# Optimization experiments

Measured on AMD Instinct MI355X. Metric: run time of the kernel, lower is better.

Reference implementation:

```python
import jax, jax.numpy as jnp
import numpy as np

N = 100000      # num_nodes
E = 1600000     # num_edges (avg degree 16)
IN = 128        # in_feats
OUT = 64        # out_feats
D = 4           # num_divisions


def setup_inputs() -> dict:
    key = jax.random.key(0)
    ks = jax.random.split(key, 6)
    feature = jax.random.normal(ks[0], (N, IN), dtype=jnp.float32)
    # per-division linear weights, stored as [D, out, in] (torch Linear layout)
    W = jax.random.normal(ks[1], (D, OUT, IN), dtype=jnp.float32) * (1.0 / np.sqrt(IN))
    norm = jax.random.uniform(ks[2], (N, 1), dtype=jnp.float32)
    src = jax.random.randint(ks[3], (E,), 0, N)
    dst = jax.random.randint(ks[4], (E,), 0, N)
    edge_div = jax.random.randint(ks[5], (E,), 0, D)
    return {"feature": feature, "W": W, "norm": norm,
            "src": src, "dst": dst, "edge_div": edge_div}


def reference(feature, W, norm, src, dst, edge_div):
    # Per-division linear transform + per-node norm scaling: [D, N, OUT]
    t = jnp.einsum('ni,doi->dno', feature, W) * norm
    # Gather the source-node features for each edge from its division's transform
    msgs = t[edge_div, src]                      # [E, OUT]
    # Scatter-sum to (dst, division) slots in one segment_sum pass
    seg = dst * D + edge_div                     # [E]
    agg = jax.ops.segment_sum(msgs, seg, num_segments=N * D)  # [N*D, OUT]
    # Row order is node-major, division-minor -> reshape == torch.cat over divisions
    h = agg.reshape(N, D * OUT) * norm           # final norm scale
    return jax.nn.relu(h)
```

## Files before the change

kernel.cpp:

```cpp
#include <hip/hip_runtime.h>


#define IN_F   128
#define OUTC   256
#define GM_ROWS 64
#define EPC    4096
#define NBMAX  512
#define STGF   5120

__device__ inline unsigned short f32_to_bf16(float f) {
    unsigned int u = __float_as_uint(f);
    unsigned int r = (u + 0x7FFFu + ((u >> 16) & 1u)) >> 16;
    return (unsigned short)r;
}
__device__ inline float bf16_to_f32(unsigned short h) {
    return __uint_as_float(((unsigned int)h) << 16);
}

__global__ __launch_bounds__(256) void transposeW_kernel(
    const float* __restrict__ W, float* __restrict__ Wt)
{
    const int idx = blockIdx.x * 256 + threadIdx.x;
    const int c = idx >> 7;
    const int k = idx & 127;
    Wt[k * OUTC + c] = W[idx];
}

__global__ __launch_bounds__(256) void gemm_kernel(
    const float* __restrict__ feat, const float* __restrict__ Wt,
    const float* __restrict__ norm, unsigned short* __restrict__ t, int nNodes)
{
    __shared__ float As[128][GM_ROWS + 4];

    const int tid = threadIdx.x;
    const int m0 = blockIdx.x * GM_ROWS;

    #pragma unroll
    for (int it = 0; it < 8; ++it) {
        const int idx = it * 1024 + tid * 4;
        const int row = idx >> 7;
        const int col = idx & 127;
        float4 v = make_float4(0.f, 0.f, 0.f, 0.f);
        const int g = m0 + row;
        if (g < nNodes) v = *(const float4*)(feat + (size_t)g * IN_F + col);
        As[col + 0][row] = v.x; As[col + 1][row] = v.y;
        As[col + 2][row] = v.z; As[col + 3][row] = v.w;
    }
    __syncthreads();

    const int tx = tid & 31;
    const int ty = tid >> 5;
    const int mb = ty * 8, nb = tx * 8;
    float acc[8][8] = {};

    #pragma unroll 4
    for (int k = 0; k < 128; ++k) {
        const float4 a0 = *(const float4*)&As[k][mb];
        const float4 a1 = *(const float4*)&As[k][mb + 4];
        const float4 b0 = *(const float4*)(Wt + k * OUTC + nb);
        const float4 b1 = *(const float4*)(Wt + k * OUTC + nb + 4);
        const float a[8] = {a0.x, a0.y, a0.z, a0.w, a1.x, a1.y, a1.z, a1.w};
        const float b[8] = {b0.x, b0.y, b0.z, b0.w, b1.x, b1.y, b1.z, b1.w};
        #pragma unroll
        for (int i = 0; i < 8; ++i)
            #pragma unroll
            for (int j = 0; j < 8; ++j)
                acc[i][j] = fmaf(a[i], b[j], acc[i][j]);
    }

    #pragma unroll
    for (int i = 0; i < 8; ++i) {
        const int gm = m0 + mb + i;
        if (gm >= nNodes) continue;
        const float nm = norm[gm];
        union { unsigned short u[8]; uint4 v; } o;
        #pragma unroll
        for (int j = 0; j < 8; ++j) o.u[j] = f32_to_bf16(acc[i][j] * nm);
        *(uint4*)(t + (size_t)gm * OUTC + nb) = o.v;
    }
}

__global__ __launch_bounds__(256) void bucket_hist_kernel(
    const int* __restrict__ dst, int* __restrict__ bcnt, int nEdges, int nBuck)
{
    __shared__ int h[NBMAX];
    const int tid = threadIdx.x;
    for (int b = tid; b < nBuck; b += 256) h[b] = 0;
    __syncthreads();
    const int e0 = blockIdx.x * EPC;
    const int cnt = min(EPC, nEdges - e0);
    for (int i = tid; i < cnt; i += 256)
        atomicAdd(&h[((unsigned)dst[e0 + i]) >> 8], 1);
    __syncthreads();
    for (int b = tid; b < nBuck; b += 256)
        if (h[b]) atomicAdd(&bcnt[b], h[b]);
}

__global__ __launch_bounds__(256) void bucket_scan_kernel(
    const int* __restrict__ bcnt, int* __restrict__ bbase,
    int* __restrict__ bfront, int nBuck)
{
    __shared__ int wsum[4], woff[4];
    const int tid = threadIdx.x;
    const int i0 = 2 * tid, i1 = 2 * tid + 1;
    const int h0 = (i0 < nBuck) ? bcnt[i0] : 0;
    const int h1 = (i1 < nBuck) ? bcnt[i1] : 0;
    const int s = h0 + h1;
    int incl = s;
    const int lane = tid & 63;
    #pragma unroll
    for (int off = 1; off < 64; off <<= 1) {
        const int o = __shfl_up(incl, off);
        if (lane >= off) incl += o;
    }
    if (lane == 63) wsum[tid >> 6] = incl;
    __syncthreads();
    if (tid == 0) { int r = 0; for (int i = 0; i < 4; ++i) { woff[i] = r; r += wsum[i]; } }
    __syncthreads();
    const int e = incl - s + woff[tid >> 6];
    if (i0 < nBuck) { bbase[i0] = e;      bfront[i0] = e;      }
    if (i1 < nBuck) { bbase[i1] = e + h0; bfront[i1] = e + h0; }
}

__global__ __launch_bounds__(256) void bucket_place_kernel(
    const int* __restrict__ src, const int* __restrict__ dst,
    const int* __restrict__ ediv, int* __restrict__ bfront,
    uint2* __restrict__ rec, int nEdges, int nBuck)
{
    __shared__ uint2 stg[EPC];
    __shared__ unsigned short stgB[EPC];
    __shared__ int hist[NBMAX], excl[NBMAX], cur[NBMAX], gpos[NBMAX];
    __shared__ int wsum[4], woff[4];

    const int tid = threadIdx.x;
    const int e0 = blockIdx.x * EPC;
    const int cnt = min(EPC, nEdges - e0);

    for (int b = tid; b < nBuck; b += 256) hist[b] = 0;
    __syncthreads();

    for (int i = tid; i < cnt; i += 256)
        atomicAdd(&hist[((unsigned)dst[e0 + i]) >> 8], 1);
    __syncthreads();

    {
        const int i0 = 2 * tid, i1 = 2 * tid + 1;
        const int h0 = (i0 < nBuck) ? hist[i0] : 0;
        const int h1 = (i1 < nBuck) ? hist[i1] : 0;
        const int s = h0 + h1;
        int incl = s;
        const int lane = tid & 63;
        #pragma unroll
        for (int off = 1; off < 64; off <<= 1) {
            const int o = __shfl_up(incl, off);
            if (lane >= off) incl += o;
        }
        if (lane == 63) wsum[tid >> 6] = incl;
        __syncthreads();
        if (tid == 0) { int r = 0; for (int i = 0; i < 4; ++i) { woff[i] = r; r += wsum[i]; } }
        __syncthreads();
        const int e = incl - s + woff[tid >> 6];
        if (i0 < nBuck) { excl[i0] = e;      cur[i0] = e;
                          gpos[i0] = h0 ? atomicAdd(&bfront[i0], h0) : 0; }
        if (i1 < nBuck) { excl[i1] = e + h0; cur[i1] = e + h0;
                          gpos[i1] = h1 ? atomicAdd(&bfront[i1], h1) : 0; }
    }
    __syncthreads();

    for (int i = tid; i < cnt; i += 256) {
        const int e = e0 + i;
        const int d = dst[e];
        const int b = ((unsigned)d) >> 8;
        const int lp = atomicAdd(&cur[b], 1);
        stg[lp]  = make_uint2((unsigned)((src[e] << 2) | ediv[e]), (unsigned)d);
        stgB[lp] = (unsigned short)b;
    }
    __syncthreads();

    for (int s2 = tid; s2 < cnt; s2 += 256) {
        const int b = stgB[s2];
        rec[gpos[b] + (s2 - excl[b])] = stg[s2];
    }
}

__global__ __launch_bounds__(256) void bucket_fine_kernel(
    const uint2* __restrict__ rec, const int* __restrict__ bbase,
    const int* __restrict__ bcnt, int* __restrict__ cursor,
    int* __restrict__ payload, int nNodes)
{
    __shared__ int nhist[256], ncur[256];
    __shared__ int pay[STGF];
    __shared__ int wsum[4], woff[4];

    const int tid = threadIdx.x;
    const int b = blockIdx.x;
    const int base = bbase[b];
    const int cnt = bcnt[b];
    const int node0 = b << 8;

    nhist[tid] = 0;
    __syncthreads();
    for (int i = tid; i < cnt; i += 256)
        atomicAdd(&nhist[rec[base + i].y & 255], 1);
    __syncthreads();

    const int v = nhist[tid];
    int incl = v;
    const int lane = tid & 63;
    #pragma unroll
    for (int off = 1; off < 64; off <<= 1) {
        const int o = __shfl_up(incl, off);
        if (lane >= off) incl += o;
    }
    if (lane == 63) wsum[tid >> 6] = incl;
    __syncthreads();
    if (tid == 0) { int r = 0; for (int i = 0; i < 4; ++i) { woff[i] = r; r += wsum[i]; } }
    __syncthreads();
    incl += woff[tid >> 6];
    ncur[tid] = incl - v;
    if (node0 + tid < nNodes) cursor[node0 + tid] = base + incl;
    __syncthreads();

    if (cnt <= STGF) {
        for (int i = tid; i < cnt; i += 256) {
            const uint2 r = rec[base + i];
            pay[atomicAdd(&ncur[r.y & 255], 1)] = (int)r.x;
        }
        __syncthreads();
        for (int i = tid; i < cnt; i += 256) payload[base + i] = pay[i];
    } else {
        for (int i = tid; i < cnt; i += 256) {
            const uint2 r = rec[base + i];
            payload[base + atomicAdd(&ncur[r.y & 255], 1)] = (int)r.x;
        }
    }
}

__global__ __launch_bounds__(256) void aggregate_kernel(
    const unsigned short* __restrict__ t, const int* __restrict__ cursor,
    const int* __restrict__ payload, const float* __restrict__ norm,
    float* __restrict__ out, int nNodes)
{
    const int wave = (int)((blockIdx.x * 256u + threadIdx.x) >> 6);
    const int lane = threadIdx.x & 63;
    if (wave >= nNodes) return;
    const int e0 = (wave == 0) ? 0 : cursor[wave - 1];
    const int e1 = cursor[wave];

    float acc0 = 0.f, acc1 = 0.f, acc2 = 0.f, acc3 = 0.f;
    int e = e0;
    for (; e + 1 < e1; e += 2) {
        const int p0 = payload[e];
        const int p1 = payload[e + 1];
        const float v0 = bf16_to_f32(t[(size_t)(p0 >> 2) * OUTC + (p0 & 3) * 64 + lane]);
        const float v1 = bf16_to_f32(t[(size_t)(p1 >> 2) * OUTC + (p1 & 3) * 64 + lane]);
        const int d0 = p0 & 3, d1 = p1 & 3;
        acc0 += (d0 == 0 ? v0 : 0.f) + (d1 == 0 ? v1 : 0.f);
        acc1 += (d0 == 1 ? v0 : 0.f) + (d1 == 1 ? v1 : 0.f);
        acc2 += (d0 == 2 ? v0 : 0.f) + (d1 == 2 ? v1 : 0.f);
        acc3 += (d0 == 3 ? v0 : 0.f) + (d1 == 3 ? v1 : 0.f);
    }
    if (e < e1) {
        const int p0 = payload[e];
        const float v0 = bf16_to_f32(t[(size_t)(p0 >> 2) * OUTC + (p0 & 3) * 64 + lane]);
        const int d0 = p0 & 3;
        acc0 += (d0 == 0 ? v0 : 0.f);
        acc1 += (d0 == 1 ? v0 : 0.f);
        acc2 += (d0 == 2 ? v0 : 0.f);
        acc3 += (d0 == 3 ? v0 : 0.f);
    }

    const float nm = norm[wave];
    float* po = out + (size_t)wave * OUTC;
    po[0 * 64 + lane] = fmaxf(acc0 * nm, 0.f);
    po[1 * 64 + lane] = fmaxf(acc1 * nm, 0.f);
    po[2 * 64 + lane] = fmaxf(acc2 * nm, 0.f);
    po[3 * 64 + lane] = fmaxf(acc3 * nm, 0.f);
}

extern "C" void kernel_launch(void* const* d_in, const int* in_sizes, int n_in,
                              void* d_out, int out_size, void* d_ws, size_t ws_size,
                              hipStream_t stream) {
    const float* feat = (const float*)d_in[0];
    const float* W    = (const float*)d_in[1];
    const float* norm = (const float*)d_in[2];
    const int*   src  = (const int*)d_in[3];
    const int*   dst  = (const int*)d_in[4];
    const int*   ediv = (const int*)d_in[5];
    float* out = (float*)d_out;

    const int nNodes = in_sizes[0] / IN_F;
    const int nEdges = in_sizes[3];
    const int nBuck  = (nNodes + 255) >> 8;
    const int nChunk = (nEdges + EPC - 1) / EPC;

    char* ws = (char*)d_ws;
    const size_t t_bytes      = (size_t)nNodes * OUTC * sizeof(unsigned short);
    const size_t rec_bytes    = (size_t)nEdges * sizeof(uint2);
    const size_t pay_bytes    = (size_t)nEdges * sizeof(int);
    const size_t cursor_bytes = (size_t)nNodes * sizeof(int);
    const size_t wt_bytes     = (size_t)IN_F * OUTC * sizeof(float);
    const size_t bk_bytes     = (size_t)NBMAX * sizeof(int);

    unsigned short* t  = (unsigned short*)ws;
    uint2* rec     = (uint2*)(ws + t_bytes);
    int*   payload = (int*)(ws + t_bytes + rec_bytes);
    int*   cursor  = (int*)(ws + t_bytes + rec_bytes + pay_bytes);
    float* Wt      = (float*)(ws + t_bytes + rec_bytes + pay_bytes + cursor_bytes);
    int*   bcnt    = (int*)(ws + t_bytes + rec_bytes + pay_bytes + cursor_bytes + wt_bytes);
    int*   bbase   = bcnt + NBMAX;
    int*   bfront  = bcnt + 2 * NBMAX;
    (void)ws_size; (void)out_size; (void)n_in; (void)bk_bytes;

    hipMemsetAsync(bcnt, 0, nBuck * sizeof(int), stream);
    transposeW_kernel<<<(IN_F * OUTC) / 256, 256, 0, stream>>>(W, Wt);
    bucket_hist_kernel<<<nChunk, 256, 0, stream>>>(dst, bcnt, nEdges, nBuck);
    bucket_scan_kernel<<<1, 256, 0, stream>>>(bcnt, bbase, bfront, nBuck);
    bucket_place_kernel<<<nChunk, 256, 0, stream>>>(src, dst, ediv, bfront, rec,
                                                    nEdges, nBuck);
    bucket_fine_kernel<<<nBuck, 256, 0, stream>>>(rec, bbase, bcnt, cursor, payload,
                                                  nNodes);
    gemm_kernel<<<(nNodes + GM_ROWS - 1) / GM_ROWS, 256, 0, stream>>>(feat, Wt, norm,
                                                                      t, nNodes);
    aggregate_kernel<<<(nNodes + 3) / 4, 256, 0, stream>>>(t, cursor, payload, norm,
                                                           out, nNodes);
}
```

Before: 399.5 us.

## Use bf16 split-precision MFMA for the transform GEMM and unroll aggregation by four

Replaces the FP32 FMA GEMM with a wave-level MFMA kernel. Feature rows and weights are each split into bf16 high and low parts, and three bf16 MFMAs per tile approximate FP32 accuracy. The weights are pre-split into hi/lo bf16 arrays instead of being transposed. The aggregation loop is also unrolled from two to four edges per iteration to expose more independent gathers. The MFMA path trades extra matrix ops and scattered 2-byte stores for matrix-core throughput.

New measurement: 371.1 us. -7.1%, faster.

```diff
diff --git a/kernel.cpp b/kernel.cpp
--- a/kernel.cpp
+++ b/kernel.cpp
@@ -3,81 +3,108 @@
 
 #define IN_F   128
 #define OUTC   256
-#define GM_ROWS 64
 #define EPC    4096
 #define NBMAX  512
 #define STGF   5120
 
-__device__ inline unsigned short f32_to_bf16(float f) {
-    unsigned int u = __float_as_uint(f);
-    unsigned int r = (u + 0x7FFFu + ((u >> 16) & 1u)) >> 16;
-    return (unsigned short)r;
-}
+typedef __bf16 bf16x8 __attribute__((ext_vector_type(8)));
+typedef float  f32x4  __attribute__((ext_vector_type(4)));
+
 __device__ inline float bf16_to_f32(unsigned short h) {
     return __uint_as_float(((unsigned int)h) << 16);
 }
 
-__global__ __launch_bounds__(256) void transposeW_kernel(
-    const float* __restrict__ W, float* __restrict__ Wt)
+__global__ __launch_bounds__(256) void wsplit_kernel(
+    const float* __restrict__ W, __bf16* __restrict__ Whi, __bf16* __restrict__ Wlo)
 {
     const int idx = blockIdx.x * 256 + threadIdx.x;
-    const int c = idx >> 7;
-    const int k = idx & 127;
-    Wt[k * OUTC + c] = W[idx];
-}
-
-__global__ __launch_bounds__(256) void gemm_kernel(
-    const float* __restrict__ feat, const float* __restrict__ Wt,
-    const float* __restrict__ norm, unsigned short* __restrict__ t, int nNodes)
-{
-    __shared__ float As[128][GM_ROWS + 4];
-
-    const int tid = threadIdx.x;
-    const int m0 = blockIdx.x * GM_ROWS;
-
-    #pragma unroll
-    for (int it = 0; it < 8; ++it) {
-        const int idx = it * 1024 + tid * 4;
-        const int row = idx >> 7;
-        const int col = idx & 127;
-        float4 v = make_float4(0.f, 0.f, 0.f, 0.f);
-        const int g = m0 + row;
-        if (g < nNodes) v = *(const float4*)(feat + (size_t)g * IN_F + col);
-        As[col + 0][row] = v.x; As[col + 1][row] = v.y;
-        As[col + 2][row] = v.z; As[col + 3][row] = v.w;
-    }
-    __syncthreads();
-
-    const int tx = tid & 31;
-    const int ty = tid >> 5;
-    const int mb = ty * 8, nb = tx * 8;
-    float acc[8][8] = {};
-
-    #pragma unroll 4
-    for (int k = 0; k < 128; ++k) {
-        const float4 a0 = *(const float4*)&As[k][mb];
-        const float4 a1 = *(const float4*)&As[k][mb + 4];
-        const float4 b0 = *(const float4*)(Wt + k * OUTC + nb);
-        const float4 b1 = *(const float4*)(Wt + k * OUTC + nb + 4);
-        const float a[8] = {a0.x, a0.y, a0.z, a0.w, a1.x, a1.y, a1.z, a1.w};
-        const float b[8] = {b0.x, b0.y, b0.z, b0.w, b1.x, b1.y, b1.z, b1.w};
-        #pragma unroll
-        for (int i = 0; i < 8; ++i)
+    const float v = W[idx];
+    const __bf16 h = (__bf16)v;
+    Whi[idx] = h;
+    Wlo[idx] = (__bf16)(v - (float)h);
+}
+
+__device__ inline void split_bf16x8(const float4 q0, const float4 q1,
+                                    bf16x8& h, bf16x8& l)
+{
+    float av[8] = {q0.x, q0.y, q0.z, q0.w, q1.x, q1.y, q1.z, q1.w};
+    #pragma unroll
+    for (int i = 0; i < 8; ++i) {
+        const __bf16 hb = (__bf16)av[i];
+        h[i] = hb;
+        l[i] = (__bf16)(av[i] - (float)hb);
+    }
+}
+
+__global__ __launch_bounds__(256) void gemm_mfma_kernel(
+    const float* __restrict__ feat, const __bf16* __restrict__ Whi,
+    const __bf16* __restrict__ Wlo, const float* __restrict__ norm,
+    __bf16* __restrict__ t, int nNodes)
+{
+    const int tid  = threadIdx.x;
+    const int wave = (blockIdx.x << 2) + (tid >> 6);
+    const int lane = tid & 63;
+    const int r    = lane & 15;
+    const int g    = lane >> 4;
+    const int row0 = wave * 32;
+    if (row0 >= nNodes) return;
+
+    f32x4 acc[2][16];
+    const f32x4 zero = {0.f, 0.f, 0.f, 0.f};
+    #pragma unroll
+    for (int h = 0; h < 2; ++h)
+        #pragma unroll
+        for (int c = 0; c < 16; ++c)
+            acc[h][c] = zero;
+
+    const int ra0 = row0 + r;
+    const int ra1 = row0 + 16 + r;
+    const float* pa0 = feat + (size_t)(ra0 < nNodes ? ra0 : 0) * IN_F;
+    const float* pa1 = feat + (size_t)(ra1 < nNodes ? ra1 : 0) * IN_F;
+    const __bf16* bhp = Whi + r * IN_F;
+    const __bf16* blp = Wlo + r * IN_F;
+
+    #pragma unroll
+    for (int s = 0; s < 4; ++s) {
+        const int koff = s * 32 + g * 8;
+        bf16x8 a0h, a0l, a1h, a1l;
+        split_bf16x8(*(const float4*)(pa0 + koff), *(const float4*)(pa0 + koff + 4),
+                     a0h, a0l);
+        split_bf16x8(*(const float4*)(pa1 + koff), *(const float4*)(pa1 + koff + 4),
+                     a1h, a1l);
+        #pragma unroll
+        for (int c = 0; c < 16; ++c) {
+            const bf16x8 bh = *(const bf16x8*)(bhp + c * 16 * IN_F + koff);
+            const bf16x8 bl = *(const bf16x8*)(blp + c * 16 * IN_F + koff);
+            acc[0][c] = __builtin_amdgcn_mfma_f32_16x16x32_bf16(a0h, bh, acc[0][c], 0, 0, 0);
+            acc[0][c] = __builtin_amdgcn_mfma_f32_16x16x32_bf16(a0l, bh, acc[0][c], 0, 0, 0);
+            acc[0][c] = __builtin_amdgcn_mfma_f32_16x16x32_bf16(a0h, bl, acc[0][c], 0, 0, 0);
+            acc[1][c] = __builtin_amdgcn_mfma_f32_16x16x32_bf16(a1h, bh, acc[1][c], 0, 0, 0);
+            acc[1][c] = __builtin_amdgcn_mfma_f32_16x16x32_bf16(a1l, bh, acc[1][c], 0, 0, 0);
+            acc[1][c] = __builtin_amdgcn_mfma_f32_16x16x32_bf16(a1h, bl, acc[1][c], 0, 0, 0);
+        }
+    }
+
+    float nv[2][4];
+    #pragma unroll
+    for (int h = 0; h < 2; ++h)
+        #pragma unroll
+        for (int j = 0; j < 4; ++j) {
+            const int grow = row0 + h * 16 + g * 4 + j;
+            nv[h][j] = (grow < nNodes) ? norm[grow] : 0.f;
+        }
+
+    #pragma unroll
+    for (int h = 0; h < 2; ++h)
+        #pragma unroll
+        for (int j = 0; j < 4; ++j) {
+            const int grow = row0 + h * 16 + g * 4 + j;
+            if (grow >= nNodes) continue;
+            __bf16* po = t + (size_t)grow * OUTC + r;
             #pragma unroll
-            for (int j = 0; j < 8; ++j)
-                acc[i][j] = fmaf(a[i], b[j], acc[i][j]);
-    }
-
-    #pragma unroll
-    for (int i = 0; i < 8; ++i) {
-        const int gm = m0 + mb + i;
-        if (gm >= nNodes) continue;
-        const float nm = norm[gm];
-        union { unsigned short u[8]; uint4 v; } o;
-        #pragma unroll
-        for (int j = 0; j < 8; ++j) o.u[j] = f32_to_bf16(acc[i][j] * nm);
-        *(uint4*)(t + (size_t)gm * OUTC + nb) = o.v;
-    }
+            for (int c = 0; c < 16; ++c)
+                po[c * 16] = (__bf16)(acc[h][c][j] * nv[h][j]);
+        }
 }
 
 __global__ __launch_bounds__(256) void bucket_hist_kernel(
@@ -223,15 +250,15 @@
 
     if (cnt <= STGF) {
         for (int i = tid; i < cnt; i += 256) {
-            const uint2 r = rec[base + i];
-            pay[atomicAdd(&ncur[r.y & 255], 1)] = (int)r.x;
+            const uint2 rr = rec[base + i];
+            pay[atomicAdd(&ncur[rr.y & 255], 1)] = (int)rr.x;
         }
         __syncthreads();
         for (int i = tid; i < cnt; i += 256) payload[base + i] = pay[i];
     } else {
         for (int i = tid; i < cnt; i += 256) {
-            const uint2 r = rec[base + i];
-            payload[base + atomicAdd(&ncur[r.y & 255], 1)] = (int)r.x;
+            const uint2 rr = rec[base + i];
+            payload[base + atomicAdd(&ncur[rr.y & 255], 1)] = (int)rr.x;
         }
     }
 }
@@ -249,18 +276,22 @@
 
     float acc0 = 0.f, acc1 = 0.f, acc2 = 0.f, acc3 = 0.f;
     int e = e0;
-    for (; e + 1 < e1; e += 2) {
-        const int p0 = payload[e];
+    for (; e + 3 < e1; e += 4) {
+        const int p0 = payload[e + 0];
         const int p1 = payload[e + 1];
+        const int p2 = payload[e + 2];
+        const int p3 = payload[e + 3];
         const float v0 = bf16_to_f32(t[(size_t)(p0 >> 2) * OUTC + (p0 & 3) * 64 + lane]);
         const float v1 = bf16_to_f32(t[(size_t)(p1 >> 2) * OUTC + (p1 & 3) * 64 + lane]);
-        const int d0 = p0 & 3, d1 = p1 & 3;
-        acc0 += (d0 == 0 ? v0 : 0.f) + (d1 == 0 ? v1 : 0.f);
-        acc1 += (d0 == 1 ? v0 : 0.f) + (d1 == 1 ? v1 : 0.f);
-        acc2 += (d0 == 2 ? v0 : 0.f) + (d1 == 2 ? v1 : 0.f);
-        acc3 += (d0 == 3 ? v0 : 0.f) + (d1 == 3 ? v1 : 0.f);
-    }
-    if (e < e1) {
+        const float v2 = bf16_to_f32(t[(size_t)(p2 >> 2) * OUTC + (p2 & 3) * 64 + lane]);
+        const float v3 = bf16_to_f32(t[(size_t)(p3 >> 2) * OUTC + (p3 & 3) * 64 + lane]);
+        const int d0 = p0 & 3, d1 = p1 & 3, d2 = p2 & 3, d3 = p3 & 3;
+        acc0 += (d0 == 0 ? v0 : 0.f) + (d1 == 0 ? v1 : 0.f) + (d2 == 0 ? v2 : 0.f) + (d3 == 0 ? v3 : 0.f);
+        acc1 += (d0 == 1 ? v0 : 0.f) + (d1 == 1 ? v1 : 0.f) + (d2 == 1 ? v2 : 0.f) + (d3 == 1 ? v3 : 0.f);
+        acc2 += (d0 == 2 ? v0 : 0.f) + (d1 == 2 ? v1 : 0.f) + (d2 == 2 ? v2 : 0.f) + (d3 == 2 ? v3 : 0.f);
+        acc3 += (d0 == 3 ? v0 : 0.f) + (d1 == 3 ? v1 : 0.f) + (d2 == 3 ? v2 : 0.f) + (d3 == 3 ? v3 : 0.f);
+    }
+    for (; e < e1; ++e) {
         const int p0 = payload[e];
         const float v0 = bf16_to_f32(t[(size_t)(p0 >> 2) * OUTC + (p0 & 3) * 64 + lane]);
         const int d0 = p0 & 3;
@@ -299,29 +330,31 @@
     const size_t rec_bytes    = (size_t)nEdges * sizeof(uint2);
     const size_t pay_bytes    = (size_t)nEdges * sizeof(int);
     const size_t cursor_bytes = (size_t)nNodes * sizeof(int);
-    const size_t wt_bytes     = (size_t)IN_F * OUTC * sizeof(float);
-    const size_t bk_bytes     = (size_t)NBMAX * sizeof(int);
-
-    unsigned short* t  = (unsigned short*)ws;
-    uint2* rec     = (uint2*)(ws + t_bytes);
-    int*   payload = (int*)(ws + t_bytes + rec_bytes);
-    int*   cursor  = (int*)(ws + t_bytes + rec_bytes + pay_bytes);
-    float* Wt      = (float*)(ws + t_bytes + rec_bytes + pay_bytes + cursor_bytes);
-    int*   bcnt    = (int*)(ws + t_bytes + rec_bytes + pay_bytes + cursor_bytes + wt_bytes);
-    int*   bbase   = bcnt + NBMAX;
-    int*   bfront  = bcnt + 2 * NBMAX;
-    (void)ws_size; (void)out_size; (void)n_in; (void)bk_bytes;
+    const size_t wsp_bytes    = (size_t)IN_F * OUTC * sizeof(__bf16);
+
+    __bf16* t      = (__bf16*)ws;
+    uint2*  rec    = (uint2*)(ws + t_bytes);
+    int*    payload= (int*)(ws + t_bytes + rec_bytes);
+    int*    cursor = (int*)(ws + t_bytes + rec_bytes + pay_bytes);
+    __bf16* Whi    = (__bf16*)(ws + t_bytes + rec_bytes + pay_bytes + cursor_bytes);
+    __bf16* Wlo    = (__bf16*)(ws + t_bytes + rec_bytes + pay_bytes + cursor_bytes + wsp_bytes);
+    int*    bcnt   = (int*)(ws + t_bytes + rec_bytes + pay_bytes + cursor_bytes + 2 * wsp_bytes);
+    int*    bbase  = bcnt + NBMAX;
+    int*    bfront = bcnt + 2 * NBMAX;
+    (void)ws_size; (void)out_size; (void)n_in;
 
     hipMemsetAsync(bcnt, 0, nBuck * sizeof(int), stream);
-    transposeW_kernel<<<(IN_F * OUTC) / 256, 256, 0, stream>>>(W, Wt);
+    wsplit_kernel<<<(IN_F * OUTC) / 256, 256, 0, stream>>>(W, Whi, Wlo);
     bucket_hist_kernel<<<nChunk, 256, 0, stream>>>(dst, bcnt, nEdges, nBuck);
     bucket_scan_kernel<<<1, 256, 0, stream>>>(bcnt, bbase, bfront, nBuck);
     bucket_place_kernel<<<nChunk, 256, 0, stream>>>(src, dst, ediv, bfront, rec,
                                                     nEdges, nBuck);
     bucket_fine_kernel<<<nBuck, 256, 0, stream>>>(rec, bbase, bcnt, cursor, payload,
                                                   nNodes);
-    gemm_kernel<<<(nNodes + GM_ROWS - 1) / GM_ROWS, 256, 0, stream>>>(feat, Wt, norm,
-                                                                      t, nNodes);
-    aggregate_kernel<<<(nNodes + 3) / 4, 256, 0, stream>>>(t, cursor, payload, norm,
+    const int gWaves  = (nNodes + 31) / 32;
+    const int gBlocks = (gWaves + 3) / 4;
+    gemm_mfma_kernel<<<gBlocks, 256, 0, stream>>>(feat, Whi, Wlo, norm, t, nNodes);
+    aggregate_kernel<<<(nNodes + 3) / 4, 256, 0, stream>>>((const unsigned short*)t,
+                                                           cursor, payload, norm,
                                                            out, nNodes);
 }
```
